# Kernel optimization log

Measured on AMD Instinct MI355X. Metric: run time of the kernel, lower is better.

## Reference

```python
import jax, jax.numpy as jnp
import numpy as np

N_ENT, D = 20000, 901
B_TR, B_TE = 100000, 25000

def setup_inputs() -> dict:
    key = jax.random.key(0)
    ks = jax.random.split(key, 12)
    feature = jax.random.normal(ks[0], (N_ENT, D), dtype=jnp.float32)
    train_sample = jax.random.randint(ks[1], (B_TR, 2), 0, N_ENT)
    test_sample = jax.random.randint(ks[2], (B_TE, 2), 0, N_ENT)
    def lin(kw, kb, fin, fout):
        bound = 1.0 / np.sqrt(fin)
        W = jax.random.uniform(kw, (fin, fout), jnp.float32, -bound, bound)
        b = jax.random.uniform(kb, (fout,), jnp.float32, -bound, bound)
        return W, b
    W1, b1 = lin(ks[3], ks[4], 2 * D, 1024)
    W2, b2 = lin(ks[5], ks[6], 1024, 512)
    W3, b3 = lin(ks[7], ks[8], 512, 64)
    W4, b4 = lin(ks[9], ks[10], 64, 1)
    return {"feature": feature, "W1": W1, "b1": b1, "W2": W2, "b2": b2,
            "W3": W3, "b3": b3, "W4": W4, "b4": b4,
            "train_sample": train_sample, "test_sample": test_sample}

def reference(feature, W1, b1, W2, b2, W3, b3, W4, b4, train_sample, test_sample):
    # vectorized replacement of the per-sample python loop: gather both rows and concat
    def mlp(pairs):
        # pairs: [B, 2] int indices -> emb [B, 2*D]
        emb = jnp.concatenate((feature[pairs[:, 0]], feature[pairs[:, 1]]), axis=1)
        # faithful to nn.Sequential: 4 stacked Linears (no inter-layer activation), Sigmoid at end
        h = emb @ W1 + b1
        h = h @ W2 + b2
        h = h @ W3 + b3
        h = h @ W4 + b4
        return jax.nn.sigmoid(h)  # [B, 1]
    return (mlp(train_sample), mlp(test_sample))
```

## Files before the change

kernel.cpp:

```cpp
#include <hip/hip_runtime.h>
#include <math.h>


#define WAVE 64

__device__ inline float wave_reduce_sum(float v) {
    #pragma unroll
    for (int off = 32; off; off >>= 1) v += __shfl_down(v, off, 64);
    return v;
}

__global__ void init_c(float* __restrict__ c, const float* __restrict__ b4) {
    *c = *b4;
}

__global__ void matvec_rows(const float* __restrict__ W,
                            const float* __restrict__ x,
                            float* __restrict__ y,
                            const float* __restrict__ bias,
                            float* __restrict__ c,
                            int M, int K) {
    int gwave = (blockIdx.x * blockDim.x + threadIdx.x) >> 6;
    int lane  = threadIdx.x & 63;
    if (gwave > M) return;
    if (gwave == M) {
        float acc = 0.f;
        for (int k = lane; k < K; k += WAVE) acc += bias[k] * x[k];
        acc = wave_reduce_sum(acc);
        if (lane == 0) atomicAdd(c, acc);
        return;
    }
    const float* row = W + (size_t)gwave * (size_t)K;
    float acc = 0.f;
    for (int k = lane; k < K; k += WAVE) acc += row[k] * x[k];
    acc = wave_reduce_sum(acc);
    if (lane == 0) y[gwave] = acc;
}

__global__ void feat_fold(const float* __restrict__ F,
                          const float* __restrict__ v1,
                          float* __restrict__ sA,
                          float* __restrict__ sB,
                          int NE, int D) {
    int gwave = (blockIdx.x * blockDim.x + threadIdx.x) >> 6;
    int lane  = threadIdx.x & 63;
    if (gwave >= NE) return;
    const float* row = F + (size_t)gwave * (size_t)D;
    const float* va  = v1;
    const float* vb  = v1 + D;
    float a = 0.f, b = 0.f;
    for (int d = lane; d < D; d += WAVE) {
        float f = row[d];
        a += f * va[d];
        b += f * vb[d];
    }
    a = wave_reduce_sum(a);
    b = wave_reduce_sum(b);
    if (lane == 0) { sA[gwave] = a; sB[gwave] = b; }
}

__global__ void head(const int* __restrict__ tr, const int* __restrict__ te,
                     const float* __restrict__ sA, const float* __restrict__ sB,
                     const float* __restrict__ c, float* __restrict__ out,
                     int ntr, int nte) {
    int i = blockIdx.x * blockDim.x + threadIdx.x;
    int n = ntr + nte;
    if (i >= n) return;
    int p0, p1;
    if (i < ntr) { p0 = tr[2 * i];          p1 = tr[2 * i + 1]; }
    else         { int j = i - ntr; p0 = te[2 * j]; p1 = te[2 * j + 1]; }
    float x = sA[p0] + sB[p1] + *c;
    out[i] = 1.0f / (1.0f + __expf(-x));
}

extern "C" void kernel_launch(void* const* d_in, const int* in_sizes, int n_in,
                              void* d_out, int out_size, void* d_ws, size_t ws_size,
                              hipStream_t stream) {
    const float* feature = (const float*)d_in[0];
    const float* W1      = (const float*)d_in[1];
    const float* b1      = (const float*)d_in[2];
    const float* W2      = (const float*)d_in[3];
    const float* b2      = (const float*)d_in[4];
    const float* W3      = (const float*)d_in[5];
    const float* b3      = (const float*)d_in[6];
    const float* W4      = (const float*)d_in[7];
    const float* b4      = (const float*)d_in[8];
    const int*   tr      = (const int*)d_in[9];
    const int*   te      = (const int*)d_in[10];
    float*       out     = (float*)d_out;

    const int NE = 20000, D = 901;
    const int NTR = in_sizes[9] / 2;
    const int NTE = in_sizes[10] / 2;

    float* ws = (float*)d_ws;
    float* v3 = ws;
    float* v2 = ws + 512;
    float* v1 = ws + 1536;
    float* c  = ws + 3338;
    float* sA = ws + 4096;
    float* sB = ws + 24096;

    init_c<<<1, 1, 0, stream>>>(c, b4);

    {
        int waves = 512 + 1;
        int blocks = (waves * 64 + 255) / 256;
        matvec_rows<<<blocks, 256, 0, stream>>>(W3, W4, v3, b3, c, 512, 64);
    }
    {
        int waves = 1024 + 1;
        int blocks = (waves * 64 + 255) / 256;
        matvec_rows<<<blocks, 256, 0, stream>>>(W2, v3, v2, b2, c, 1024, 512);
    }
    {
        int waves = 1802 + 1;
        int blocks = (waves * 64 + 255) / 256;
        matvec_rows<<<blocks, 256, 0, stream>>>(W1, v2, v1, b1, c, 1802, 1024);
    }
    {
        int waves = NE;
        int blocks = (waves * 64 + 255) / 256;
        feat_fold<<<blocks, 256, 0, stream>>>(feature, v1, sA, sB, NE, D);
    }
    {
        int n = NTR + NTE;
        int blocks = (n + 255) / 256;
        head<<<blocks, 256, 0, stream>>>(tr, te, sA, sB, c, out, NTR, NTE);
    }
}
```

Measured before the change: 152.8 us.

## Fuse all stages into one cooperative persistent kernel with vectorized loads

Replaces the five separate launches (init, three mat-vec folds, feature fold, head) with a single cooperative kernel of 512 blocks that runs each stage in turn, separated by grid-wide syncs. Mat-vec rows and feature rows are read with float4 loads, with alignment peeling for the 901-wide feature rows. The folded v1 coefficients are kept in registers across a grid-stride loop over entity rows. The aim is to cut launch and inter-kernel gaps and to raise load efficiency. In exchange it pays for the grid syncs and keeps a multi-kernel fallback in case cooperative launch fails.

```diff
diff --git a/kernel.cpp b/kernel.cpp
--- a/kernel.cpp
+++ b/kernel.cpp
@@ -1,8 +1,12 @@
 #include <hip/hip_runtime.h>
+#include <hip/hip_cooperative_groups.h>
 #include <math.h>
 
-
-#define WAVE 64
+namespace cg = cooperative_groups;
+
+
+#define NBLK 512
+#define NTHR 256
 
 __device__ inline float wave_reduce_sum(float v) {
     #pragma unroll
@@ -10,122 +14,227 @@
     return v;
 }
 
-__global__ void init_c(float* __restrict__ c, const float* __restrict__ b4) {
-    *c = *b4;
-}
-
-__global__ void matvec_rows(const float* __restrict__ W,
-                            const float* __restrict__ x,
-                            float* __restrict__ y,
-                            const float* __restrict__ bias,
-                            float* __restrict__ c,
-                            int M, int K) {
-    int gwave = (blockIdx.x * blockDim.x + threadIdx.x) >> 6;
-    int lane  = threadIdx.x & 63;
-    if (gwave > M) return;
-    if (gwave == M) {
-        float acc = 0.f;
-        for (int k = lane; k < K; k += WAVE) acc += bias[k] * x[k];
-        acc = wave_reduce_sum(acc);
-        if (lane == 0) atomicAdd(c, acc);
-        return;
-    }
-    const float* row = W + (size_t)gwave * (size_t)K;
-    float acc = 0.f;
-    for (int k = lane; k < K; k += WAVE) acc += row[k] * x[k];
-    acc = wave_reduce_sum(acc);
-    if (lane == 0) y[gwave] = acc;
-}
-
-__global__ void feat_fold(const float* __restrict__ F,
-                          const float* __restrict__ v1,
-                          float* __restrict__ sA,
-                          float* __restrict__ sB,
-                          int NE, int D) {
-    int gwave = (blockIdx.x * blockDim.x + threadIdx.x) >> 6;
-    int lane  = threadIdx.x & 63;
-    if (gwave >= NE) return;
-    const float* row = F + (size_t)gwave * (size_t)D;
-    const float* va  = v1;
-    const float* vb  = v1 + D;
-    float a = 0.f, b = 0.f;
-    for (int d = lane; d < D; d += WAVE) {
-        float f = row[d];
-        a += f * va[d];
-        b += f * vb[d];
-    }
-    a = wave_reduce_sum(a);
-    b = wave_reduce_sum(b);
-    if (lane == 0) { sA[gwave] = a; sB[gwave] = b; }
-}
-
-__global__ void head(const int* __restrict__ tr, const int* __restrict__ te,
-                     const float* __restrict__ sA, const float* __restrict__ sB,
-                     const float* __restrict__ c, float* __restrict__ out,
-                     int ntr, int nte) {
-    int i = blockIdx.x * blockDim.x + threadIdx.x;
-    int n = ntr + nte;
-    if (i >= n) return;
-    int p0, p1;
-    if (i < ntr) { p0 = tr[2 * i];          p1 = tr[2 * i + 1]; }
-    else         { int j = i - ntr; p0 = te[2 * j]; p1 = te[2 * j + 1]; }
-    float x = sA[p0] + sB[p1] + *c;
-    out[i] = 1.0f / (1.0f + __expf(-x));
+__device__ inline void stageA(const float* __restrict__ W3, const float* __restrict__ b3,
+                              const float* __restrict__ W4, const float* __restrict__ b4,
+                              float* __restrict__ v3, float* __restrict__ c,
+                              int gwave, int lane) {
+    if (gwave > 512) return;
+    float x = W4[lane];
+    if (gwave == 512) {
+        float acc = wave_reduce_sum(b3[lane] * x);
+        if (lane == 0) *c = *b4 + acc;
+    } else {
+        float acc = wave_reduce_sum(W3[(size_t)gwave * 64 + lane] * x);
+        if (lane == 0) v3[gwave] = acc;
+    }
+}
+
+__device__ inline void stageB(const float* __restrict__ W2, const float* __restrict__ b2,
+                              const float* __restrict__ v3, float* __restrict__ v2,
+                              float* __restrict__ c, int gwave, int lane) {
+    if (gwave > 1024) return;
+    if (gwave == 1024) {
+        float acc = 0.f;
+        for (int k = lane; k < 512; k += 64) acc += b2[k] * v3[k];
+        acc = wave_reduce_sum(acc);
+        if (lane == 0) *c += acc;
+    } else {
+        const float4* row4 = (const float4*)(W2 + (size_t)gwave * 512);
+        const float4* x4   = (const float4*)v3;
+        float acc = 0.f;
+        #pragma unroll
+        for (int it = 0; it < 2; ++it) {
+            float4 w = row4[lane + 64 * it];
+            float4 x = x4[lane + 64 * it];
+            acc += w.x * x.x + w.y * x.y + w.z * x.z + w.w * x.w;
+        }
+        acc = wave_reduce_sum(acc);
+        if (lane == 0) v2[gwave] = acc;
+    }
+}
+
+__device__ inline void stageC(const float* __restrict__ W1, const float* __restrict__ b1,
+                              const float* __restrict__ v2, float* __restrict__ v1,
+                              float* __restrict__ c, int gwave, int lane) {
+    if (gwave > 1802) return;
+    if (gwave == 1802) {
+        float acc = 0.f;
+        for (int k = lane; k < 1024; k += 64) acc += b1[k] * v2[k];
+        acc = wave_reduce_sum(acc);
+        if (lane == 0) *c += acc;
+    } else {
+        const float4* row4 = (const float4*)(W1 + (size_t)gwave * 1024);
+        const float4* x4   = (const float4*)v2;
+        float acc = 0.f;
+        #pragma unroll
+        for (int it = 0; it < 4; ++it) {
+            float4 w = row4[lane + 64 * it];
+            float4 x = x4[lane + 64 * it];
+            acc += w.x * x.x + w.y * x.y + w.z * x.z + w.w * x.w;
+        }
+        acc = wave_reduce_sum(acc);
+        if (lane == 0) v1[gwave] = acc;
+    }
+}
+
+__device__ inline void stageD(const float* __restrict__ F, const float* __restrict__ v1,
+                              float* __restrict__ sA, float* __restrict__ sB,
+                              int NE, int D, int gwave, int lane, int nwave) {
+    const float* va = v1;
+    const float* vb = v1 + D;
+    const int a0   = (4 - (gwave & 3)) & 3;
+    const int nvec = (D - a0) >> 2;
+    const int rem  = (D - a0) & 3;
+
+    float ca[16], cb[16];
+    #pragma unroll
+    for (int it = 0; it < 4; ++it) {
+        int vi = lane + 64 * it;
+        int d  = a0 + 4 * vi;
+        bool ok = vi < nvec;
+        ca[4*it+0] = ok ? va[d+0] : 0.f;  cb[4*it+0] = ok ? vb[d+0] : 0.f;
+        ca[4*it+1] = ok ? va[d+1] : 0.f;  cb[4*it+1] = ok ? vb[d+1] : 0.f;
+        ca[4*it+2] = ok ? va[d+2] : 0.f;  cb[4*it+2] = ok ? vb[d+2] : 0.f;
+        ca[4*it+3] = ok ? va[d+3] : 0.f;  cb[4*it+3] = ok ? vb[d+3] : 0.f;
+    }
+    float cpa = (lane < a0) ? va[lane] : 0.f;
+    float cpb = (lane < a0) ? vb[lane] : 0.f;
+    int   dt  = a0 + 4 * nvec + lane;
+    float cta = (lane < rem) ? va[dt] : 0.f;
+    float ctb = (lane < rem) ? vb[dt] : 0.f;
+
+    for (int row = gwave; row < NE; row += nwave) {
+        const float* p = F + (size_t)row * (size_t)D;
+        float a = 0.f, b = 0.f;
+        if (lane < a0) { float f = p[lane]; a = f * cpa; b = f * cpb; }
+        const float4* p4 = (const float4*)(p + a0);
+        #pragma unroll
+        for (int it = 0; it < 4; ++it) {
+            int vi = lane + 64 * it;
+            if (vi < nvec) {
+                float4 f = p4[vi];
+                a += f.x * ca[4*it+0] + f.y * ca[4*it+1]
+                   + f.z * ca[4*it+2] + f.w * ca[4*it+3];
+                b += f.x * cb[4*it+0] + f.y * cb[4*it+1]
+                   + f.z * cb[4*it+2] + f.w * cb[4*it+3];
+            }
+        }
+        if (lane < rem) { float f = p[a0 + 4 * nvec + lane]; a += f * cta; b += f * ctb; }
+        a = wave_reduce_sum(a);
+        b = wave_reduce_sum(b);
+        if (lane == 0) { sA[row] = a; sB[row] = b; }
+    }
+}
+
+__device__ inline void stageE(const int* __restrict__ tr, const int* __restrict__ te,
+                              const float* __restrict__ sA, const float* __restrict__ sB,
+                              const float* __restrict__ c, float* __restrict__ out,
+                              int NTR, int NTE, int tid, int nthreads) {
+    const float cc = *c;
+    const int n = NTR + NTE;
+    for (int i = tid; i < n; i += nthreads) {
+        int2 pr;
+        if (i < NTR) pr = ((const int2*)tr)[i];
+        else         pr = ((const int2*)te)[i - NTR];
+        float x = sA[pr.x] + sB[pr.y] + cc;
+        out[i] = 1.0f / (1.0f + __expf(-x));
+    }
+}
+
+__global__ __launch_bounds__(NTHR, 2)
+void fused(const float* __restrict__ F,
+           const float* __restrict__ W1, const float* __restrict__ b1,
+           const float* __restrict__ W2, const float* __restrict__ b2,
+           const float* __restrict__ W3, const float* __restrict__ b3,
+           const float* __restrict__ W4, const float* __restrict__ b4,
+           const int* __restrict__ tr, const int* __restrict__ te,
+           float* __restrict__ out, float* __restrict__ ws,
+           int NE, int D, int NTR, int NTE)
+{
+    cg::grid_group grid = cg::this_grid();
+    float* v3 = ws;       float* v2 = ws + 512;  float* v1 = ws + 1536;
+    float* c  = ws + 3400; float* sA = ws + 4096; float* sB = ws + 24096;
+
+    const int tid      = blockIdx.x * blockDim.x + threadIdx.x;
+    const int nthreads = gridDim.x * blockDim.x;
+    const int gwave    = tid >> 6;
+    const int nwave    = nthreads >> 6;
+    const int lane     = tid & 63;
+
+    stageA(W3, b3, W4, b4, v3, c, gwave, lane);
+    grid.sync();
+    stageB(W2, b2, v3, v2, c, gwave, lane);
+    grid.sync();
+    stageC(W1, b1, v2, v1, c, gwave, lane);
+    grid.sync();
+    stageD(F, v1, sA, sB, NE, D, gwave, lane, nwave);
+    grid.sync();
+    stageE(tr, te, sA, sB, c, out, NTR, NTE, tid, nthreads);
+}
+
+__global__ __launch_bounds__(NTHR, 2)
+void kA(const float* W3, const float* b3, const float* W4, const float* b4,
+        float* v3, float* c) {
+    int tid = blockIdx.x * blockDim.x + threadIdx.x;
+    stageA(W3, b3, W4, b4, v3, c, tid >> 6, tid & 63);
+}
+__global__ __launch_bounds__(NTHR, 2)
+void kB(const float* W2, const float* b2, const float* v3, float* v2, float* c) {
+    int tid = blockIdx.x * blockDim.x + threadIdx.x;
+    stageB(W2, b2, v3, v2, c, tid >> 6, tid & 63);
+}
+__global__ __launch_bounds__(NTHR, 2)
+void kC(const float* W1, const float* b1, const float* v2, float* v1, float* c) {
+    int tid = blockIdx.x * blockDim.x + threadIdx.x;
+    stageC(W1, b1, v2, v1, c, tid >> 6, tid & 63);
+}
+__global__ __launch_bounds__(NTHR, 2)
+void kD(const float* F, const float* v1, float* sA, float* sB, int NE, int D) {
+    int tid = blockIdx.x * blockDim.x + threadIdx.x;
+    stageD(F, v1, sA, sB, NE, D, tid >> 6, tid & 63, (gridDim.x * blockDim.x) >> 6);
+}
+__global__ __launch_bounds__(NTHR, 2)
+void kE(const int* tr, const int* te, const float* sA, const float* sB,
+        const float* c, float* out, int NTR, int NTE) {
+    int tid = blockIdx.x * blockDim.x + threadIdx.x;
+    stageE(tr, te, sA, sB, c, out, NTR, NTE, tid, gridDim.x * blockDim.x);
 }
 
 extern "C" void kernel_launch(void* const* d_in, const int* in_sizes, int n_in,
                               void* d_out, int out_size, void* d_ws, size_t ws_size,
                               hipStream_t stream) {
-    const float* feature = (const float*)d_in[0];
-    const float* W1      = (const float*)d_in[1];
-    const float* b1      = (const float*)d_in[2];
-    const float* W2      = (const float*)d_in[3];
-    const float* b2      = (const float*)d_in[4];
-    const float* W3      = (const float*)d_in[5];
-    const float* b3      = (const float*)d_in[6];
-    const float* W4      = (const float*)d_in[7];
-    const float* b4      = (const float*)d_in[8];
-    const int*   tr      = (const int*)d_in[9];
-    const int*   te      = (const int*)d_in[10];
-    float*       out     = (float*)d_out;
-
-    const int NE = 20000, D = 901;
-    const int NTR = in_sizes[9] / 2;
-    const int NTE = in_sizes[10] / 2;
-
-    float* ws = (float*)d_ws;
-    float* v3 = ws;
-    float* v2 = ws + 512;
-    float* v1 = ws + 1536;
-    float* c  = ws + 3338;
-    float* sA = ws + 4096;
-    float* sB = ws + 24096;
-
-    init_c<<<1, 1, 0, stream>>>(c, b4);
-
-    {
-        int waves = 512 + 1;
-        int blocks = (waves * 64 + 255) / 256;
-        matvec_rows<<<blocks, 256, 0, stream>>>(W3, W4, v3, b3, c, 512, 64);
-    }
-    {
-        int waves = 1024 + 1;
-        int blocks = (waves * 64 + 255) / 256;
-        matvec_rows<<<blocks, 256, 0, stream>>>(W2, v3, v2, b2, c, 1024, 512);
-    }
-    {
-        int waves = 1802 + 1;
-        int blocks = (waves * 64 + 255) / 256;
-        matvec_rows<<<blocks, 256, 0, stream>>>(W1, v2, v1, b1, c, 1802, 1024);
-    }
-    {
-        int waves = NE;
-        int blocks = (waves * 64 + 255) / 256;
-        feat_fold<<<blocks, 256, 0, stream>>>(feature, v1, sA, sB, NE, D);
-    }
-    {
-        int n = NTR + NTE;
-        int blocks = (n + 255) / 256;
-        head<<<blocks, 256, 0, stream>>>(tr, te, sA, sB, c, out, NTR, NTE);
-    }
-}
+    const float* F  = (const float*)d_in[0];
+    const float* W1 = (const float*)d_in[1];
+    const float* b1 = (const float*)d_in[2];
+    const float* W2 = (const float*)d_in[3];
+    const float* b2 = (const float*)d_in[4];
+    const float* W3 = (const float*)d_in[5];
+    const float* b3 = (const float*)d_in[6];
+    const float* W4 = (const float*)d_in[7];
+    const float* b4 = (const float*)d_in[8];
+    const int*   tr = (const int*)d_in[9];
+    const int*   te = (const int*)d_in[10];
+    float*       out = (float*)d_out;
+    float*       ws  = (float*)d_ws;
+
+    int NE = 20000, D = 901;
+    int NTR = in_sizes[9] / 2;
+    int NTE = in_sizes[10] / 2;
+
+    void* args[] = { (void*)&F, (void*)&W1, (void*)&b1, (void*)&W2, (void*)&b2,
+                     (void*)&W3, (void*)&b3, (void*)&W4, (void*)&b4,
+                     (void*)&tr, (void*)&te, (void*)&out, (void*)&ws,
+                     (void*)&NE, (void*)&D, (void*)&NTR, (void*)&NTE };
+    hipError_t err = hipLaunchCooperativeKernel((const void*)fused, dim3(NBLK),
+                                                dim3(NTHR), args, 0, stream);
+    if (err != hipSuccess) {
+        (void)hipGetLastError();
+        float* v3 = ws;        float* v2 = ws + 512;  float* v1 = ws + 1536;
+        float* c  = ws + 3400; float* sA = ws + 4096; float* sB = ws + 24096;
+        kA<<<129, NTHR, 0, stream>>>(W3, b3, W4, b4, v3, c);
+        kB<<<257, NTHR, 0, stream>>>(W2, b2, v3, v2, c);
+        kC<<<451, NTHR, 0, stream>>>(W1, b1, v2, v1, c);
+        kD<<<NBLK, NTHR, 0, stream>>>(F, v1, sA, sB, NE, D);
+        kE<<<NBLK, NTHR, 0, stream>>>(tr, te, sA, sB, c, out, NTR, NTE);
+    }
+}
```

Result: slower. 386.6 us (+153.0%).
